# Performance work log

Hardware: AMD Instinct MI355X
Metric: run time of the kernel (lower is better)

## Reference

```python
import jax, jax.numpy as jnp
import numpy as np

N_REF, PHRASE_LEN, ASCII = 50000, 32, 128
BATCH = 16


def setup_inputs() -> dict:
    key = jax.random.key(0)
    k1, k2 = jax.random.split(key)
    x = jax.random.normal(k1, (BATCH, PHRASE_LEN, ASCII), dtype=jnp.float32)
    raw_phrases = jax.random.normal(k2, (N_REF, PHRASE_LEN, ASCII), dtype=jnp.float32)
    return {"x": x, "raw_phrases": raw_phrases}


def reference(x, raw_phrases):
    # dist[b, n] = sum_{l,a} (raw_phrases[n,l,a] - x[b,l,a])**2
    # Expanded form avoids materializing the [B, N, L, A] difference tensor
    # (which would be ~13 GB); exact same math up to fp reassociation.
    r2 = jnp.sum(raw_phrases * raw_phrases, axis=(1, 2))          # [N]
    x2 = jnp.sum(x * x, axis=(1, 2))                              # [B]
    xr = jnp.einsum('bla,nla->bn', x, raw_phrases)                # [B, N]
    dist = r2[None, :] - 2.0 * xr + x2[:, None]                   # [B, N]
    # torch F.softmax on a 1-D tensor (no dim) softmaxes over the reference axis.
    # Note: the original applies softmax to the (positive) distances directly.
    return jax.nn.softmax(dist, axis=-1)                          # [B, N]
```

## Files before the change

### kernel.cpp

```cpp
#include <hip/hip_runtime.h>
#include <math.h>

#define N_REF   50000
#define BATCH   16
#define KDIM    4096
#define CHUNK   256
#define NCHUNK  (KDIM / CHUNK)
#define RPB     16
#define RPW     4

__global__ __launch_bounds__(256) void dist_kernel(const float* __restrict__ x,
                                                   const float* __restrict__ raw,
                                                   float* __restrict__ dist)
{
    __shared__ float xs[BATCH * CHUNK];
    const int tid  = threadIdx.x;
    const int lane = tid & 63;
    const int wv   = tid >> 6;
    const long n_base = (long)blockIdx.x * RPB + wv * RPW;

    float acc[BATCH][RPW];
    #pragma unroll
    for (int b = 0; b < BATCH; ++b)
        #pragma unroll
        for (int r = 0; r < RPW; ++r) acc[b][r] = 0.f;
    float r2a[RPW] = {0.f, 0.f, 0.f, 0.f};

    for (int c = 0; c < NCHUNK; ++c) {
        __syncthreads();
        #pragma unroll
        for (int i = 0; i < 4; ++i) {
            const int slot = i * 256 + tid;
            const int b = slot >> 6;
            const int f = slot & 63;
            const float4 v = *(const float4*)(x + (size_t)b * KDIM + (size_t)c * CHUNK + f * 4);
            *(float4*)(xs + b * CHUNK + f * 4) = v;
        }
        __syncthreads();

        float4 rv[RPW];
        #pragma unroll
        for (int r = 0; r < RPW; ++r) {
            rv[r] = *(const float4*)(raw + (size_t)(n_base + r) * KDIM
                                         + (size_t)c * CHUNK + lane * 4);
            r2a[r] = fmaf(rv[r].x, rv[r].x, r2a[r]);
            r2a[r] = fmaf(rv[r].y, rv[r].y, r2a[r]);
            r2a[r] = fmaf(rv[r].z, rv[r].z, r2a[r]);
            r2a[r] = fmaf(rv[r].w, rv[r].w, r2a[r]);
        }
        #pragma unroll
        for (int b = 0; b < BATCH; ++b) {
            const float4 xv = *(const float4*)(xs + b * CHUNK + lane * 4);
            #pragma unroll
            for (int r = 0; r < RPW; ++r) {
                acc[b][r] = fmaf(rv[r].x, xv.x, acc[b][r]);
                acc[b][r] = fmaf(rv[r].y, xv.y, acc[b][r]);
                acc[b][r] = fmaf(rv[r].z, xv.z, acc[b][r]);
                acc[b][r] = fmaf(rv[r].w, xv.w, acc[b][r]);
            }
        }
    }

    float vals[64];
    #pragma unroll
    for (int b = 0; b < BATCH; ++b)
        #pragma unroll
        for (int r = 0; r < RPW; ++r) vals[b * RPW + r] = acc[b][r];

    #pragma unroll
    for (int k = 0; k < 6; ++k) {
        const int bit = 1 << k;
        const bool hi = (lane & bit) != 0;
        #pragma unroll
        for (int i = 0; i < (64 >> (k + 1)); ++i) {
            const float a  = vals[2 * i];
            const float bb = vals[2 * i + 1];
            const float keep = hi ? bb : a;
            const float send = hi ? a  : bb;
            const float recv = __shfl_xor(send, bit, 64);
            vals[i] = keep + recv;
        }
    }

    #pragma unroll
    for (int r = 0; r < RPW; ++r) {
        #pragma unroll
        for (int k = 0; k < 6; ++k)
            r2a[r] += __shfl_xor(r2a[r], 1 << k, 64);
    }

    const int b_out = lane >> 2;
    const int r_out = lane & 3;
    const float r2v = (r_out == 0) ? r2a[0] : (r_out == 1) ? r2a[1]
                    : (r_out == 2) ? r2a[2] : r2a[3];
    dist[(size_t)b_out * N_REF + (size_t)(n_base + r_out)] = r2v - 2.0f * vals[0];
}

__global__ __launch_bounds__(1024) void softmax_kernel(float* __restrict__ d)
{
    const int b = blockIdx.x;
    float* row = d + (size_t)b * N_REF;
    const int tid = threadIdx.x;

    float m = -INFINITY, s = 0.f;
    for (int n = tid; n < N_REF; n += 1024) {
        const float v = row[n];
        const float M = fmaxf(m, v);
        s = s * __expf(m - M) + __expf(v - M);
        m = M;
    }
    #pragma unroll
    for (int k = 1; k < 64; k <<= 1) {
        const float mo = __shfl_xor(m, k, 64);
        const float so = __shfl_xor(s, k, 64);
        const float M  = fmaxf(m, mo);
        s = s * __expf(m - M) + so * __expf(mo - M);
        m = M;
    }
    __shared__ float ms[16], ss[16];
    const int wv = tid >> 6, lane = tid & 63;
    if (lane == 0) { ms[wv] = m; ss[wv] = s; }
    __syncthreads();
    if (tid == 0) {
        float M = ms[0], S = ss[0];
        for (int i = 1; i < 16; ++i) {
            const float M2 = fmaxf(M, ms[i]);
            S = S * __expf(M - M2) + ss[i] * __expf(ms[i] - M2);
            M = M2;
        }
        ms[0] = M; ss[0] = 1.f / S;
    }
    __syncthreads();
    const float M = ms[0], Sinv = ss[0];
    for (int n = tid; n < N_REF; n += 1024)
        row[n] = __expf(row[n] - M) * Sinv;
}

extern "C" void kernel_launch(void* const* d_in, const int* in_sizes, int n_in,
                              void* d_out, int out_size, void* d_ws, size_t ws_size,
                              hipStream_t stream) {
    const float* x   = (const float*)d_in[0];
    const float* raw = (const float*)d_in[1];
    float* out = (float*)d_out;

    dist_kernel<<<N_REF / RPB, 256, 0, stream>>>(x, raw, out);
    softmax_kernel<<<BATCH, 1024, 0, stream>>>(out);
}
```

Baseline: 221.9 us.

## Double-buffer GEMV tiles with async LDS loads and split softmax across blocks

The distance kernel now double-buffers the x chunk in shared memory, filling it with global_load_lds async copies, and prefetches the next chunk's reference rows into registers while computing the current one. Work is remapped so each wave covers 8 batches by 8 rows instead of 16 by 4, and occupancy is hinted with launch bounds. The softmax, previously 16 blocks each walking a whole row, is split into a partial max/sum pass and a normalize pass over 25x16 blocks. The split is meant to fix the softmax's poor parallelism. It costs an extra launch, a workspace buffer and more register pressure in the distance kernel.

```diff
diff --git a/kernel.cpp b/kernel.cpp
--- a/kernel.cpp
+++ b/kernel.cpp
@@ -7,65 +7,97 @@
 #define CHUNK   256
 #define NCHUNK  (KDIM / CHUNK)
 #define RPB     16
-#define RPW     4
-
-__global__ __launch_bounds__(256) void dist_kernel(const float* __restrict__ x,
-                                                   const float* __restrict__ raw,
-                                                   float* __restrict__ dist)
+#define BH      8
+#define RW      8
+
+typedef __attribute__((address_space(3))) uint32_t lds_u32;
+typedef const __attribute__((address_space(1))) uint32_t glb_u32;
+
+__global__ __launch_bounds__(256, 3) void dist_kernel(const float* __restrict__ x,
+                                                      const float* __restrict__ raw,
+                                                      float* __restrict__ dist)
 {
-    __shared__ float xs[BATCH * CHUNK];
+    __shared__ float xs[2][BATCH * CHUNK];
     const int tid  = threadIdx.x;
     const int lane = tid & 63;
     const int wv   = tid >> 6;
-    const long n_base = (long)blockIdx.x * RPB + wv * RPW;
-
-    float acc[BATCH][RPW];
-    #pragma unroll
-    for (int b = 0; b < BATCH; ++b)
-        #pragma unroll
-        for (int r = 0; r < RPW; ++r) acc[b][r] = 0.f;
-    float r2a[RPW] = {0.f, 0.f, 0.f, 0.f};
-
-    for (int c = 0; c < NCHUNK; ++c) {
+    const int bb   = (wv & 1) * BH;
+    const long rowbase = (long)blockIdx.x * RPB + (long)(wv >> 1) * RW;
+
+    float acc[BH][RW];
+    #pragma unroll
+    for (int bi = 0; bi < BH; ++bi)
+        #pragma unroll
+        for (int r = 0; r < RW; ++r) acc[bi][r] = 0.f;
+    float r2a[RW];
+    #pragma unroll
+    for (int r = 0; r < RW; ++r) r2a[r] = 0.f;
+
+    float4 rvA[RW], rvB[RW];
+
+#define STAGE(buf, c) do {                                                      \
+        _Pragma("unroll")                                                       \
+        for (int i_ = 0; i_ < 4; ++i_) {                                        \
+            const int b_ = i_ * 4 + wv;                                         \
+            const float* g_ = x + (size_t)b_ * KDIM + (size_t)(c) * CHUNK + lane * 4; \
+            const float* l_ = &xs[buf][b_ * CHUNK];                             \
+            __builtin_amdgcn_global_load_lds((glb_u32*)g_, (lds_u32*)l_, 16, 0, 0); \
+        }                                                                       \
+    } while (0)
+
+#define LOADRV(dst, c) do {                                                     \
+        _Pragma("unroll")                                                       \
+        for (int r_ = 0; r_ < RW; ++r_)                                         \
+            dst[r_] = *(const float4*)(raw + (size_t)(rowbase + r_) * KDIM      \
+                                           + (size_t)(c) * CHUNK + lane * 4);   \
+    } while (0)
+
+#define COMPUTE(rv, buf) do {                                                   \
+        _Pragma("unroll")                                                       \
+        for (int r_ = 0; r_ < RW; ++r_) {                                       \
+            r2a[r_] = fmaf(rv[r_].x, rv[r_].x, r2a[r_]);                        \
+            r2a[r_] = fmaf(rv[r_].y, rv[r_].y, r2a[r_]);                        \
+            r2a[r_] = fmaf(rv[r_].z, rv[r_].z, r2a[r_]);                        \
+            r2a[r_] = fmaf(rv[r_].w, rv[r_].w, r2a[r_]);                        \
+        }                                                                       \
+        _Pragma("unroll")                                                       \
+        for (int bi_ = 0; bi_ < BH; ++bi_) {                                    \
+            const float4 xv_ = *(const float4*)(&xs[buf][(bb + bi_) * CHUNK + lane * 4]); \
+            _Pragma("unroll")                                                   \
+            for (int r_ = 0; r_ < RW; ++r_) {                                   \
+                acc[bi_][r_] = fmaf(rv[r_].x, xv_.x, acc[bi_][r_]);             \
+                acc[bi_][r_] = fmaf(rv[r_].y, xv_.y, acc[bi_][r_]);             \
+                acc[bi_][r_] = fmaf(rv[r_].z, xv_.z, acc[bi_][r_]);             \
+                acc[bi_][r_] = fmaf(rv[r_].w, xv_.w, acc[bi_][r_]);             \
+            }                                                                   \
+        }                                                                       \
+    } while (0)
+
+    STAGE(0, 0);
+    LOADRV(rvA, 0);
+    __syncthreads();
+
+    for (int cc = 0; cc < NCHUNK / 2 - 1; ++cc) {
+        STAGE(1, 2 * cc + 1);
+        LOADRV(rvB, 2 * cc + 1);
+        COMPUTE(rvA, 0);
         __syncthreads();
-        #pragma unroll
-        for (int i = 0; i < 4; ++i) {
-            const int slot = i * 256 + tid;
-            const int b = slot >> 6;
-            const int f = slot & 63;
-            const float4 v = *(const float4*)(x + (size_t)b * KDIM + (size_t)c * CHUNK + f * 4);
-            *(float4*)(xs + b * CHUNK + f * 4) = v;
-        }
+        STAGE(0, 2 * cc + 2);
+        LOADRV(rvA, 2 * cc + 2);
+        COMPUTE(rvB, 1);
         __syncthreads();
-
-        float4 rv[RPW];
-        #pragma unroll
-        for (int r = 0; r < RPW; ++r) {
-            rv[r] = *(const float4*)(raw + (size_t)(n_base + r) * KDIM
-                                         + (size_t)c * CHUNK + lane * 4);
-            r2a[r] = fmaf(rv[r].x, rv[r].x, r2a[r]);
-            r2a[r] = fmaf(rv[r].y, rv[r].y, r2a[r]);
-            r2a[r] = fmaf(rv[r].z, rv[r].z, r2a[r]);
-            r2a[r] = fmaf(rv[r].w, rv[r].w, r2a[r]);
-        }
-        #pragma unroll
-        for (int b = 0; b < BATCH; ++b) {
-            const float4 xv = *(const float4*)(xs + b * CHUNK + lane * 4);
-            #pragma unroll
-            for (int r = 0; r < RPW; ++r) {
-                acc[b][r] = fmaf(rv[r].x, xv.x, acc[b][r]);
-                acc[b][r] = fmaf(rv[r].y, xv.y, acc[b][r]);
-                acc[b][r] = fmaf(rv[r].z, xv.z, acc[b][r]);
-                acc[b][r] = fmaf(rv[r].w, xv.w, acc[b][r]);
-            }
-        }
-    }
+    }
+    STAGE(1, NCHUNK - 1);
+    LOADRV(rvB, NCHUNK - 1);
+    COMPUTE(rvA, 0);
+    __syncthreads();
+    COMPUTE(rvB, 1);
 
     float vals[64];
     #pragma unroll
-    for (int b = 0; b < BATCH; ++b)
-        #pragma unroll
-        for (int r = 0; r < RPW; ++r) vals[b * RPW + r] = acc[b][r];
+    for (int bi = 0; bi < BH; ++bi)
+        #pragma unroll
+        for (int r = 0; r < RW; ++r) vals[bi * RW + r] = acc[bi][r];
 
     #pragma unroll
     for (int k = 0; k < 6; ++k) {
@@ -74,40 +106,56 @@
         #pragma unroll
         for (int i = 0; i < (64 >> (k + 1)); ++i) {
             const float a  = vals[2 * i];
-            const float bb = vals[2 * i + 1];
-            const float keep = hi ? bb : a;
-            const float send = hi ? a  : bb;
+            const float bbv = vals[2 * i + 1];
+            const float keep = hi ? bbv : a;
+            const float send = hi ? a   : bbv;
             const float recv = __shfl_xor(send, bit, 64);
             vals[i] = keep + recv;
         }
     }
 
     #pragma unroll
-    for (int r = 0; r < RPW; ++r) {
+    for (int r = 0; r < RW; ++r) {
         #pragma unroll
         for (int k = 0; k < 6; ++k)
             r2a[r] += __shfl_xor(r2a[r], 1 << k, 64);
     }
 
-    const int b_out = lane >> 2;
-    const int r_out = lane & 3;
-    const float r2v = (r_out == 0) ? r2a[0] : (r_out == 1) ? r2a[1]
-                    : (r_out == 2) ? r2a[2] : r2a[3];
-    dist[(size_t)b_out * N_REF + (size_t)(n_base + r_out)] = r2v - 2.0f * vals[0];
-}
-
-__global__ __launch_bounds__(1024) void softmax_kernel(float* __restrict__ d)
+    const int rsel = lane & 7;
+    float r2v = r2a[0];
+    if (rsel == 1) r2v = r2a[1];
+    if (rsel == 2) r2v = r2a[2];
+    if (rsel == 3) r2v = r2a[3];
+    if (rsel == 4) r2v = r2a[4];
+    if (rsel == 5) r2v = r2a[5];
+    if (rsel == 6) r2v = r2a[6];
+    if (rsel == 7) r2v = r2a[7];
+
+    const int b_out = bb + (lane >> 3);
+    dist[(size_t)b_out * N_REF + (size_t)(rowbase + rsel)] = r2v - 2.0f * vals[0];
+}
+
+#define SMB   25
+#define SMC   2000
+
+__global__ __launch_bounds__(256) void softmax_part(const float* __restrict__ d,
+                                                    float2* __restrict__ part)
 {
-    const int b = blockIdx.x;
-    float* row = d + (size_t)b * N_REF;
+    const int row = blockIdx.y, cb = blockIdx.x;
+    const float* p = d + (size_t)row * N_REF + (size_t)cb * SMC;
     const int tid = threadIdx.x;
 
     float m = -INFINITY, s = 0.f;
-    for (int n = tid; n < N_REF; n += 1024) {
-        const float v = row[n];
-        const float M = fmaxf(m, v);
-        s = s * __expf(m - M) + __expf(v - M);
-        m = M;
+    #pragma unroll
+    for (int i = 0; i < 2; ++i) {
+        const int q = tid + i * 256;
+        if (q < SMC / 4) {
+            const float4 v = *(const float4*)(p + q * 4);
+            const float M = fmaxf(m, fmaxf(fmaxf(v.x, v.y), fmaxf(v.z, v.w)));
+            s = s * __expf(m - M) + __expf(v.x - M) + __expf(v.y - M)
+                                  + __expf(v.z - M) + __expf(v.w - M);
+            m = M;
+        }
     }
     #pragma unroll
     for (int k = 1; k < 64; k <<= 1) {
@@ -117,23 +165,51 @@
         s = s * __expf(m - M) + so * __expf(mo - M);
         m = M;
     }
-    __shared__ float ms[16], ss[16];
+    __shared__ float2 wsum[4];
     const int wv = tid >> 6, lane = tid & 63;
-    if (lane == 0) { ms[wv] = m; ss[wv] = s; }
+    if (lane == 0) wsum[wv] = make_float2(m, s);
     __syncthreads();
     if (tid == 0) {
-        float M = ms[0], S = ss[0];
-        for (int i = 1; i < 16; ++i) {
-            const float M2 = fmaxf(M, ms[i]);
-            S = S * __expf(M - M2) + ss[i] * __expf(ms[i] - M2);
+        float M = wsum[0].x, S = wsum[0].y;
+        #pragma unroll
+        for (int i = 1; i < 4; ++i) {
+            const float M2 = fmaxf(M, wsum[i].x);
+            S = S * __expf(M - M2) + wsum[i].y * __expf(wsum[i].x - M2);
             M = M2;
         }
-        ms[0] = M; ss[0] = 1.f / S;
-    }
-    __syncthreads();
-    const float M = ms[0], Sinv = ss[0];
-    for (int n = tid; n < N_REF; n += 1024)
-        row[n] = __expf(row[n] - M) * Sinv;
+        part[row * SMB + cb] = make_float2(M, S);
+    }
+}
+
+__global__ __launch_bounds__(256) void softmax_norm(float* __restrict__ d,
+                                                    const float2* __restrict__ part)
+{
+    const int row = blockIdx.y, cb = blockIdx.x;
+    const int tid = threadIdx.x;
+
+    float M = -INFINITY, S = 0.f;
+    #pragma unroll
+    for (int i = 0; i < SMB; ++i) {
+        const float2 ps = part[row * SMB + i];
+        const float M2 = fmaxf(M, ps.x);
+        S = S * __expf(M - M2) + ps.y * __expf(ps.x - M2);
+        M = M2;
+    }
+    const float Sinv = 1.f / S;
+
+    float* p = d + (size_t)row * N_REF + (size_t)cb * SMC;
+    #pragma unroll
+    for (int i = 0; i < 2; ++i) {
+        const int q = tid + i * 256;
+        if (q < SMC / 4) {
+            float4 v = *(float4*)(p + q * 4);
+            v.x = __expf(v.x - M) * Sinv;
+            v.y = __expf(v.y - M) * Sinv;
+            v.z = __expf(v.z - M) * Sinv;
+            v.w = __expf(v.w - M) * Sinv;
+            *(float4*)(p + q * 4) = v;
+        }
+    }
 }
 
 extern "C" void kernel_launch(void* const* d_in, const int* in_sizes, int n_in,
@@ -142,7 +218,9 @@
     const float* x   = (const float*)d_in[0];
     const float* raw = (const float*)d_in[1];
     float* out = (float*)d_out;
+    float2* part = (float2*)d_ws;
 
     dist_kernel<<<N_REF / RPB, 256, 0, stream>>>(x, raw, out);
-    softmax_kernel<<<BATCH, 1024, 0, stream>>>(out);
-}
+    softmax_part<<<dim3(SMB, BATCH), 256, 0, stream>>>(out, part);
+    softmax_norm<<<dim3(SMB, BATCH), 256, 0, stream>>>(out, part);
+}
```

After: 523.9 us. +136.1%, slower.
